# Kernel tuning notes

Measured on AMD Instinct MI355X. Metric: run time of the kernel, lower is better.

## Reference

```python
import jax, jax.numpy as jnp
import numpy as np

B, S, D, H = 4, 2048, 256, 4
DH = D // H  # per-head dim (shared for q, k, v)


def setup_inputs() -> dict:
    key = jax.random.key(0)
    ks = jax.random.split(key, 10)
    scale = 1.0 / np.sqrt(D)
    return {
        "q": jax.random.normal(ks[0], (B, S, D), jnp.float32),
        "k": jax.random.normal(ks[1], (B, S, D), jnp.float32),
        "v": jax.random.normal(ks[2], (B, S, D), jnp.float32),
        "mask": jax.random.randint(ks[3], (B, S, S), 0, 2).astype(bool),
        # per-head query/key projections: [H, D, DH] (+ bias [H, DH])
        "Wq": jax.random.uniform(ks[4], (H, D, DH), jnp.float32, -scale, scale),
        "bq": jax.random.uniform(ks[5], (H, DH), jnp.float32, -scale, scale),
        "Wk": jax.random.uniform(ks[6], (H, D, DH), jnp.float32, -scale, scale),
        "bk": jax.random.uniform(ks[7], (H, DH), jnp.float32, -scale, scale),
        # shared value projection: [D, DH]
        "Wv": jax.random.uniform(ks[8], (D, DH), jnp.float32, -scale, scale),
        "bv": jnp.zeros((DH,), jnp.float32),
        # final projection (no bias): [DH, D]
        "Wf": jax.random.uniform(ks[9], (DH, D), jnp.float32, -scale, scale),
    }


def reference(q, k, v, mask, Wq, bq, Wk, bk, Wv, bv, Wf):
    # per-head projections (all heads at once): [B, H, S, DH]
    q_h = jnp.einsum("bsd,hde->bhse", q, Wq) + bq[None, :, None, :]
    k_h = jnp.einsum("bsd,hde->bhse", k, Wk) + bk[None, :, None, :]
    # shared value projection: [B, S, DH]
    v_p = v @ Wv + bv
    # scaled scores: [B, H, S, S]
    scores = jnp.einsum("bhse,bhte->bhst", q_h, k_h) / jnp.sqrt(
        jnp.asarray(DH, q_h.dtype)
    )
    scores = jnp.where(mask[:, None, :, :], jnp.asarray(-1e9, scores.dtype), scores)
    attn = jax.nn.softmax(scores, axis=-1)  # [B, H, S, S]
    # shared V for every head: [B, H, S, DH]
    heads = jnp.einsum("bhst,bte->bhse", attn, v_p)
    mean_head = heads.mean(axis=1)  # [B, S, DH]
    out = mean_head @ Wf  # [B, S, D]
    return out, attn
```

## Files before the change

### kernel.cpp

```cpp
#include <hip/hip_runtime.h>
#include <stdint.h>
#include <stddef.h>

#define B_ 4
#define S_ 2048
#define D_ 256
#define H_ 4
#define DH_ 64
#define NT 128
#define SC_LOG2E 0.18033688011112042f

typedef __attribute__((ext_vector_type(8))) short short8;
typedef __attribute__((ext_vector_type(4))) short short4v;
typedef __attribute__((ext_vector_type(4))) float f32x4;
typedef unsigned int uint;

__device__ __forceinline__ short bf16_rne(float f) {
  union { float f; uint32_t u; } c; c.f = f;
  uint32_t u = c.u + 0x7FFFu + ((c.u >> 16) & 1u);
  return (short)(u >> 16);
}

__device__ __forceinline__ f32x4 mfma16(short8 a, short8 b, f32x4 c) {
  return __builtin_amdgcn_mfma_f32_16x16x32_bf16(a, b, c, 0, 0, 0);
}

__device__ __forceinline__ void gl_lds16(const short* g, short* l) {
  __builtin_amdgcn_global_load_lds(
      (const __attribute__((address_space(1))) unsigned int*)g,
      (__attribute__((address_space(3))) unsigned int*)l, 16, 0, 0);
}

__global__ void prep_weights(const float* __restrict__ Wq, const float* __restrict__ Wk,
                             const float* __restrict__ Wv,
                             short* __restrict__ WqT, short* __restrict__ WkT,
                             short* __restrict__ WvT) {
  int tid = blockIdx.x * blockDim.x + threadIdx.x;
  if (tid < 65536) {
    int n = tid >> 8, d = tid & 255;
    int hh = n >> 6, e = n & 63;
    WqT[tid] = bf16_rne(Wq[((size_t)hh * D_ + d) * DH_ + e]);
    WkT[tid] = bf16_rne(Wk[((size_t)hh * D_ + d) * DH_ + e]);
  } else if (tid < 65536 + 16384) {
    int t2 = tid - 65536;
    int e = t2 >> 8, d = t2 & 255;
    WvT[t2] = bf16_rne(Wv[(size_t)d * DH_ + e]);
  }
}

__global__ void detect_kernel(const unsigned int* __restrict__ m, int* __restrict__ flag) {
  __shared__ int isbool;
  if (threadIdx.x == 0) isbool = 0;
  __syncthreads();
#pragma unroll
  for (int i = 0; i < 4; ++i) {
    unsigned int d = m[threadIdx.x + i * 256];
    if (d & 0xFFFFFFFEu) isbool = 1;
  }
  __syncthreads();
  if (threadIdx.x == 0) *flag = isbool ? 0 : 1;
}

__global__ __launch_bounds__(256) void pack_mask(const unsigned char* __restrict__ maskB,
                                                 const int* __restrict__ flagp,
                                                 uint* __restrict__ mbits) {
  int tid = blockIdx.x * 256 + threadIdx.x;
  uint w = 0;
  if (*flagp) {
    const uint4* p = (const uint4*)((const uint*)maskB + (size_t)tid * 32);
#pragma unroll
    for (int i = 0; i < 8; ++i) {
      uint4 d = p[i];
      w |= (d.x ? 1u : 0u) << (i * 4);
      w |= (d.y ? 1u : 0u) << (i * 4 + 1);
      w |= (d.z ? 1u : 0u) << (i * 4 + 2);
      w |= (d.w ? 1u : 0u) << (i * 4 + 3);
    }
  } else {
    const uint4* p = (const uint4*)(maskB + (size_t)tid * 32);
#pragma unroll
    for (int i = 0; i < 2; ++i) {
      uint4 d = p[i];
      const uint* dw = (const uint*)&d;
#pragma unroll
      for (int j = 0; j < 4; ++j) {
        uint x = dw[j];
        int base = i * 16 + j * 4;
        w |= ((x & 0x000000FFu) ? 1u : 0u) << (base);
        w |= ((x & 0x0000FF00u) ? 1u : 0u) << (base + 1);
        w |= ((x & 0x00FF0000u) ? 1u : 0u) << (base + 2);
        w |= ((x & 0xFF000000u) ? 1u : 0u) << (base + 3);
      }
    }
  }
  mbits[tid] = w;
}

__global__ __launch_bounds__(256) void proj_kernel(
    const float* __restrict__ X, const short* __restrict__ WT,
    const float* __restrict__ bias, short* __restrict__ outp, int vmode) {
  const int b = blockIdx.z;
  const int s0 = blockIdx.x * 64;
  const int n0 = blockIdx.y * 64;
  const int tid = threadIdx.x;
  const int wave = tid >> 6, lane = tid & 63;
  const int lr = lane & 15, lg = lane >> 4;

  const int arowi = s0 + wave * 16 + lr;
  const float* xr = X + ((size_t)b * S_ + arowi) * D_;

  f32x4 zero4 = {0.f, 0.f, 0.f, 0.f};
  f32x4 acc[4];
#pragma unroll
  for (int ct = 0; ct < 4; ++ct) acc[ct] = zero4;

#pragma unroll
  for (int c = 0; c < 8; ++c) {
    const int k0 = c * 32 + lg * 8;
    f32x4 x0 = *(const f32x4*)(xr + k0);
    f32x4 x1 = *(const f32x4*)(xr + k0 + 4);
    short8 a;
#pragma unroll
    for (int jj = 0; jj < 4; ++jj) { a[jj] = bf16_rne(x0[jj]); a[4 + jj] = bf16_rne(x1[jj]); }
#pragma unroll
    for (int ct = 0; ct < 4; ++ct) {
      short8 bw = *(const short8*)(WT + (size_t)(n0 + ct * 16 + lr) * D_ + k0);
      acc[ct] = mfma16(a, bw, acc[ct]);
    }
  }

  if (vmode == 0) {
#pragma unroll
    for (int ct = 0; ct < 4; ++ct) {
      int n = n0 + ct * 16 + lr;
      float bb = bias[n];
      int hh = n >> 6, e = n & 63;
#pragma unroll
      for (int r = 0; r < 4; ++r) {
        int srow = s0 + wave * 16 + lg * 4 + r;
        outp[(((size_t)b * H_ + hh) * S_ + srow) * DH_ + e] = bf16_rne(acc[ct][r] + bb);
      }
    }
  } else {
#pragma unroll
    for (int ct = 0; ct < 4; ++ct) {
      int n = n0 + ct * 16 + lr;
      float bb = bias[n];
      int s4 = s0 + wave * 16 + lg * 4;
      short4v pk;
#pragma unroll
      for (int r = 0; r < 4; ++r) pk[r] = bf16_rne(acc[ct][r] + bb);
      *(short4v*)(outp + ((size_t)b * DH_ + n) * S_ + s4) = pk;
    }
  }
}

__device__ __forceinline__ void stageK(const short* Ksrc, short* dst, int wave, int lane) {
#pragma unroll
  for (int i = 0; i < 4; ++i) {
    int db = i * 256 + wave * 64;
    int d = db + lane;
    int s = (d & ~7) | ((d ^ (d >> 3)) & 7);
    gl_lds16(Ksrc + (size_t)s * 8, dst + (size_t)db * 8);
  }
}

__device__ __forceinline__ void stageV(const short* Vb, int t0, short* dst, int wave, int lane) {
#pragma unroll
  for (int i = 0; i < 4; ++i) {
    int db = i * 256 + wave * 64;
    int d = db + lane;
    int s = (d & ~15) | ((d ^ (d >> 4)) & 15);
    int er = s >> 4, c16 = s & 15;
    gl_lds16(Vb + (size_t)er * S_ + t0 + c16 * 8, dst + (size_t)db * 8);
  }
}

__global__ __launch_bounds__(256) void attn_kernel(
    const short* __restrict__ qh, const short* __restrict__ kh,
    const short* __restrict__ vT, const uint* __restrict__ mbits,
    float* __restrict__ attn, float* __restrict__ heads) {
  __shared__ __align__(16) short Kt[2][NT][DH_];
  __shared__ __align__(16) short Vt[2][DH_][NT];
  __shared__ __align__(16) short Pt[4][16][NT];

  const int flat = blockIdx.x;
  const int xcd = flat & 7;
  const int pos = flat >> 3;
  const int bh_i = xcd * 2 + (pos >> 5);
  const int q0 = (pos & 31) * 64;
  const int b = bh_i >> 2, h = bh_i & 3;

  const int tid = threadIdx.x;
  const int wave = tid >> 6, lane = tid & 63;
  const int lr = lane & 15, lg = lane >> 4;

  const size_t bh = (size_t)b * H_ + h;
  const short* Qb = qh + bh * S_ * DH_;
  const short* Kb = kh + bh * S_ * DH_;
  const short* Vb = vT + (size_t)b * DH_ * S_;

  const int qrow = q0 + wave * 16 + lr;
  const uint* mrow = mbits + ((size_t)b * S_ + qrow) * (S_ / 32);
  float* arow = attn + (bh * S_ + qrow) * S_;

  short8 aq0 = *(const short8*)(Qb + (size_t)qrow * DH_ + lg * 8);
  short8 aq1 = *(const short8*)(Qb + (size_t)qrow * DH_ + 32 + lg * 8);

  short* pw = &Pt[wave][0][0];

  float rsum = 0.f;
  stageK(Kb, &Kt[0][0][0], wave, lane);
  __syncthreads();
  int cur = 0;
  for (int t0 = 0; t0 < S_; t0 += NT) {
    if (t0 + NT < S_) stageK(Kb + (size_t)(t0 + NT) * DH_, &Kt[cur ^ 1][0][0], wave, lane);
    const short* kt = &Kt[cur][0][0];
    uint4 mv = *(const uint4*)(mrow + (t0 >> 5));
#pragma unroll
    for (int j = 0; j < 8; ++j) {
      int row = j * 16 + lr;
      int rs = row & 7;
      short8 bk0 = *(const short8*)(kt + row * 64 + ((lg ^ rs) * 8));
      short8 bk1 = *(const short8*)(kt + row * 64 + (((lg + 4) ^ rs) * 8));
      f32x4 acc = {0.f, 0.f, 0.f, 0.f};
      acc = mfma16(bk0, aq0, acc);
      acc = mfma16(bk1, aq1, acc);
      uint mw = ((const uint*)&mv)[j >> 1];
#pragma unroll
      for (int r = 0; r < 4; ++r) {
        int sh = (j & 1) * 16 + lg * 4 + r;
        float p = ((mw >> sh) & 1u) ? 0.f : __builtin_exp2f(acc[r] * SC_LOG2E);
        rsum += p;
      }
    }
    __syncthreads();
    cur ^= 1;
  }
  rsum += __shfl_xor(rsum, 16);
  rsum += __shfl_xor(rsum, 32);
  const float rinv = 1.0f / rsum;

  f32x4 o[4];
#pragma unroll
  for (int ct = 0; ct < 4; ++ct) o[ct] = (f32x4){0.f, 0.f, 0.f, 0.f};

  stageK(Kb, &Kt[0][0][0], wave, lane);
  stageV(Vb, 0, &Vt[0][0][0], wave, lane);
  __syncthreads();
  cur = 0;
  for (int t0 = 0; t0 < S_; t0 += NT) {
    if (t0 + NT < S_) {
      stageK(Kb + (size_t)(t0 + NT) * DH_, &Kt[cur ^ 1][0][0], wave, lane);
      stageV(Vb, t0 + NT, &Vt[cur ^ 1][0][0], wave, lane);
    }
    const short* kt = &Kt[cur][0][0];
    const short* vt = &Vt[cur][0][0];
    uint4 mv = *(const uint4*)(mrow + (t0 >> 5));
#pragma unroll
    for (int j = 0; j < 8; ++j) {
      int row = j * 16 + lr;
      int rs = row & 7;
      short8 bk0 = *(const short8*)(kt + row * 64 + ((lg ^ rs) * 8));
      short8 bk1 = *(const short8*)(kt + row * 64 + (((lg + 4) ^ rs) * 8));
      f32x4 acc = {0.f, 0.f, 0.f, 0.f};
      acc = mfma16(bk0, aq0, acc);
      acc = mfma16(bk1, aq1, acc);
      uint mw = ((const uint*)&mv)[j >> 1];
      f32x4 pst;
      short4v pk;
#pragma unroll
      for (int r = 0; r < 4; ++r) {
        int sh = (j & 1) * 16 + lg * 4 + r;
        float p = ((mw >> sh) & 1u) ? 0.f : __builtin_exp2f(acc[r] * SC_LOG2E) * rinv;
        pst[r] = p;
        pk[r] = bf16_rne(p);
      }
      *(f32x4*)(arow + t0 + j * 16 + lg * 4) = pst;
      int slot = j * 2 + (lg >> 1);
      *(short4v*)(pw + lr * 128 + ((slot ^ lr) * 8) + (lg & 1) * 4) = pk;
    }
#pragma unroll
    for (int ct = 0; ct < 4; ++ct) {
#pragma unroll
      for (int kc = 0; kc < 4; ++kc) {
        short8 apf = *(const short8*)(pw + lr * 128 + (((kc * 4 + lg) ^ lr) * 8));
        int er = ct * 16 + lr;
        short8 bvf = *(const short8*)(vt + er * 128 + (((kc * 4 + lg) ^ (er & 15)) * 8));
        o[ct] = mfma16(bvf, apf, o[ct]);
      }
    }
    __syncthreads();
    cur ^= 1;
  }

#pragma unroll
  for (int ct = 0; ct < 4; ++ct)
    *(f32x4*)(heads + (bh * S_ + qrow) * DH_ + ct * 16 + lg * 4) = o[ct];
}

__global__ __launch_bounds__(256) void final_kernel(
    const float* __restrict__ heads, const float* __restrict__ Wf,
    float* __restrict__ outp) {
  __shared__ float mean[16][DH_];
  const int row0 = blockIdx.x * 16;
  const int tid = threadIdx.x;
#pragma unroll
  for (int i = 0; i < 4; ++i) {
    int idx = tid + i * 256;
    int r = idx >> 6, e = idx & 63;
    int gs = row0 + r;
    int bb = gs >> 11, ss = gs & (S_ - 1);
    float acc = 0.f;
#pragma unroll
    for (int hh = 0; hh < H_; ++hh)
      acc += heads[(((size_t)bb * H_ + hh) * S_ + ss) * DH_ + e];
    mean[r][e] = acc * 0.25f;
  }
  __syncthreads();
  float acc[16];
#pragma unroll
  for (int r = 0; r < 16; ++r) acc[r] = 0.f;
  for (int e = 0; e < DH_; ++e) {
    float wf = Wf[(size_t)e * D_ + tid];
#pragma unroll
    for (int r = 0; r < 16; ++r) acc[r] += mean[r][e] * wf;
  }
#pragma unroll
  for (int r = 0; r < 16; ++r)
    outp[(size_t)(row0 + r) * D_ + tid] = acc[r];
}

extern "C" void kernel_launch(void* const* d_in, const int* in_sizes, int n_in,
                              void* d_out, int out_size, void* d_ws, size_t ws_size,
                              hipStream_t stream) {
  (void)in_sizes; (void)n_in; (void)out_size; (void)ws_size;
  const float* q  = (const float*)d_in[0];
  const float* k  = (const float*)d_in[1];
  const float* v  = (const float*)d_in[2];
  const unsigned char* mask = (const unsigned char*)d_in[3];
  const float* Wq = (const float*)d_in[4];
  const float* bq = (const float*)d_in[5];
  const float* Wk = (const float*)d_in[6];
  const float* bk = (const float*)d_in[7];
  const float* Wv = (const float*)d_in[8];
  const float* bv = (const float*)d_in[9];
  const float* Wf = (const float*)d_in[10];

  float* out  = (float*)d_out;
  float* attn = out + (size_t)B_ * S_ * D_;

  char* ws = (char*)d_ws;
  short* qh    = (short*)(ws);
  short* kh    = (short*)(ws + 4194304);
  short* vT    = (short*)(ws + 8388608);
  short* WqT   = (short*)(ws + 9437184);
  short* WkT   = (short*)(ws + 9568256);
  short* WvT   = (short*)(ws + 9699328);
  float* heads = (float*)(ws + 9732096);
  int*   flag  = (int*)(ws + 18120704);
  uint*  mbits = (uint*)(ws + 18120768);

  detect_kernel<<<1, 256, 0, stream>>>((const unsigned int*)mask, flag);
  pack_mask<<<2048, 256, 0, stream>>>(mask, flag, mbits);
  prep_weights<<<320, 256, 0, stream>>>(Wq, Wk, Wv, WqT, WkT, WvT);
  proj_kernel<<<dim3(32, 4, B_), 256, 0, stream>>>(q, WqT, bq, qh, 0);
  proj_kernel<<<dim3(32, 4, B_), 256, 0, stream>>>(k, WkT, bk, kh, 0);
  proj_kernel<<<dim3(32, 1, B_), 256, 0, stream>>>(v, WvT, bv, vT, 1);
  attn_kernel<<<512, 256, 0, stream>>>(qh, kh, vT, mbits, attn, heads);
  final_kernel<<<512, 256, 0, stream>>>(heads, Wf, out);
}
```

Measured before the change: 182.7 us.

## Split attention key range across two wave groups and fold softmax scale into Wq

The attention kernel now launches 512 threads per block. Two groups of four waves each handle one half of the key sequence with 64-wide tiles, then combine their row sums and output accumulators through LDS. The softmax scale times log2(e) is folded into the Q weights and bias, which removes one multiply per score. This raises the number of waves per query block, giving more latency hiding for the exp and global attention-write work, at the cost of extra syncs and an LDS reduction. Rounding Q to bf16 after the scale is applied slightly changes numerics.

```diff
diff --git a/kernel.cpp b/kernel.cpp
--- a/kernel.cpp
+++ b/kernel.cpp
@@ -7,7 +7,7 @@
 #define D_ 256
 #define H_ 4
 #define DH_ 64
-#define NT 128
+#define NTT 64
 #define SC_LOG2E 0.18033688011112042f
 
 typedef __attribute__((ext_vector_type(8))) short short8;
@@ -39,7 +39,7 @@
   if (tid < 65536) {
     int n = tid >> 8, d = tid & 255;
     int hh = n >> 6, e = n & 63;
-    WqT[tid] = bf16_rne(Wq[((size_t)hh * D_ + d) * DH_ + e]);
+    WqT[tid] = bf16_rne(Wq[((size_t)hh * D_ + d) * DH_ + e] * SC_LOG2E);
     WkT[tid] = bf16_rne(Wk[((size_t)hh * D_ + d) * DH_ + e]);
   } else if (tid < 65536 + 16384) {
     int t2 = tid - 65536;
@@ -98,7 +98,7 @@
 
 __global__ __launch_bounds__(256) void proj_kernel(
     const float* __restrict__ X, const short* __restrict__ WT,
-    const float* __restrict__ bias, short* __restrict__ outp, int vmode) {
+    const float* __restrict__ bias, short* __restrict__ outp, int vmode, float bscale) {
   const int b = blockIdx.z;
   const int s0 = blockIdx.x * 64;
   const int n0 = blockIdx.y * 64;
@@ -133,7 +133,7 @@
 #pragma unroll
     for (int ct = 0; ct < 4; ++ct) {
       int n = n0 + ct * 16 + lr;
-      float bb = bias[n];
+      float bb = bias[n] * bscale;
       int hh = n >> 6, e = n & 63;
 #pragma unroll
       for (int r = 0; r < 4; ++r) {
@@ -155,34 +155,33 @@
   }
 }
 
-__device__ __forceinline__ void stageK(const short* Ksrc, short* dst, int wave, int lane) {
-#pragma unroll
-  for (int i = 0; i < 4; ++i) {
-    int db = i * 256 + wave * 64;
-    int d = db + lane;
-    int s = (d & ~7) | ((d ^ (d >> 3)) & 7);
-    gl_lds16(Ksrc + (size_t)s * 8, dst + (size_t)db * 8);
-  }
-}
-
-__device__ __forceinline__ void stageV(const short* Vb, int t0, short* dst, int wave, int lane) {
-#pragma unroll
-  for (int i = 0; i < 4; ++i) {
-    int db = i * 256 + wave * 64;
-    int d = db + lane;
-    int s = (d & ~15) | ((d ^ (d >> 4)) & 15);
-    int er = s >> 4, c16 = s & 15;
-    gl_lds16(Vb + (size_t)er * S_ + t0 + c16 * 8, dst + (size_t)db * 8);
-  }
-}
-
-__global__ __launch_bounds__(256) void attn_kernel(
+__device__ __forceinline__ void stageK64(const short* Ksrc, short* dst, int wq, int lane) {
+#pragma unroll
+  for (int i = 0; i < 2; ++i) {
+    int ub = i * 256 + wq * 64;
+    int u = ub + lane;
+    int row = u >> 3, c = (u ^ row) & 7;
+    gl_lds16(Ksrc + (size_t)row * 64 + c * 8, dst + (size_t)ub * 8);
+  }
+}
+
+__device__ __forceinline__ void stageV64(const short* Vb, int t0, short* dst, int wq, int lane) {
+#pragma unroll
+  for (int i = 0; i < 2; ++i) {
+    int ub = i * 256 + wq * 64;
+    int u = ub + lane;
+    int er = u >> 3, c = (u ^ er) & 7;
+    gl_lds16(Vb + (size_t)er * S_ + t0 + c * 8, dst + (size_t)ub * 8);
+  }
+}
+
+__global__ __launch_bounds__(512, 4) void attn_kernel(
     const short* __restrict__ qh, const short* __restrict__ kh,
     const short* __restrict__ vT, const uint* __restrict__ mbits,
     float* __restrict__ attn, float* __restrict__ heads) {
-  __shared__ __align__(16) short Kt[2][NT][DH_];
-  __shared__ __align__(16) short Vt[2][DH_][NT];
-  __shared__ __align__(16) short Pt[4][16][NT];
+  __shared__ __align__(16) short Kt[2][2][4096];
+  __shared__ __align__(16) short Vt[2][2][4096];
+  __shared__ __align__(16) short Pt[8][1024];
 
   const int flat = blockIdx.x;
   const int xcd = flat & 7;
@@ -193,44 +192,46 @@
 
   const int tid = threadIdx.x;
   const int wave = tid >> 6, lane = tid & 63;
+  const int half = wave >> 2, wq = wave & 3;
   const int lr = lane & 15, lg = lane >> 4;
+  const int tbase = half * (S_ / 2);
 
   const size_t bh = (size_t)b * H_ + h;
   const short* Qb = qh + bh * S_ * DH_;
   const short* Kb = kh + bh * S_ * DH_;
   const short* Vb = vT + (size_t)b * DH_ * S_;
 
-  const int qrow = q0 + wave * 16 + lr;
+  const int qrow = q0 + wq * 16 + lr;
   const uint* mrow = mbits + ((size_t)b * S_ + qrow) * (S_ / 32);
   float* arow = attn + (bh * S_ + qrow) * S_;
 
-  short8 aq0 = *(const short8*)(Qb + (size_t)qrow * DH_ + lg * 8);
-  short8 aq1 = *(const short8*)(Qb + (size_t)qrow * DH_ + 32 + lg * 8);
-
-  short* pw = &Pt[wave][0][0];
+  const short8 aq0 = *(const short8*)(Qb + (size_t)qrow * DH_ + lg * 8);
+  const short8 aq1 = *(const short8*)(Qb + (size_t)qrow * DH_ + 32 + lg * 8);
+
+  short* pw = &Pt[wave][0];
 
   float rsum = 0.f;
-  stageK(Kb, &Kt[0][0][0], wave, lane);
+  stageK64(Kb + (size_t)tbase * DH_, Kt[half][0], wq, lane);
   __syncthreads();
   int cur = 0;
-  for (int t0 = 0; t0 < S_; t0 += NT) {
-    if (t0 + NT < S_) stageK(Kb + (size_t)(t0 + NT) * DH_, &Kt[cur ^ 1][0][0], wave, lane);
-    const short* kt = &Kt[cur][0][0];
-    uint4 mv = *(const uint4*)(mrow + (t0 >> 5));
-#pragma unroll
-    for (int j = 0; j < 8; ++j) {
+  for (int tt = 0; tt < 16; ++tt) {
+    const int t0 = tbase + tt * NTT;
+    if (tt + 1 < 16) stageK64(Kb + (size_t)(t0 + NTT) * DH_, Kt[half][cur ^ 1], wq, lane);
+    const short* kt = Kt[half][cur];
+    uint2 mv = *(const uint2*)(mrow + (t0 >> 5));
+#pragma unroll
+    for (int j = 0; j < 4; ++j) {
       int row = j * 16 + lr;
-      int rs = row & 7;
-      short8 bk0 = *(const short8*)(kt + row * 64 + ((lg ^ rs) * 8));
-      short8 bk1 = *(const short8*)(kt + row * 64 + (((lg + 4) ^ rs) * 8));
+      short8 bk0 = *(const short8*)(kt + row * 64 + (((lg) ^ row) & 7) * 8);
+      short8 bk1 = *(const short8*)(kt + row * 64 + (((lg + 4) ^ row) & 7) * 8);
       f32x4 acc = {0.f, 0.f, 0.f, 0.f};
       acc = mfma16(bk0, aq0, acc);
       acc = mfma16(bk1, aq1, acc);
-      uint mw = ((const uint*)&mv)[j >> 1];
+      uint mw = (j < 2) ? mv.x : mv.y;
 #pragma unroll
       for (int r = 0; r < 4; ++r) {
         int sh = (j & 1) * 16 + lg * 4 + r;
-        float p = ((mw >> sh) & 1u) ? 0.f : __builtin_exp2f(acc[r] * SC_LOG2E);
+        float p = ((mw >> sh) & 1u) ? 0.f : __builtin_exp2f(acc[r]);
         rsum += p;
       }
     }
@@ -239,64 +240,82 @@
   }
   rsum += __shfl_xor(rsum, 16);
   rsum += __shfl_xor(rsum, 32);
-  const float rinv = 1.0f / rsum;
+  float* fsum = (float*)&Pt[0][0];
+  if (lane < 16) fsum[wave * 16 + lr] = rsum;
+  __syncthreads();
+  const float rinv = 1.0f / (fsum[wq * 16 + lr] + fsum[(wq + 4) * 16 + lr]);
 
   f32x4 o[4];
 #pragma unroll
   for (int ct = 0; ct < 4; ++ct) o[ct] = (f32x4){0.f, 0.f, 0.f, 0.f};
 
-  stageK(Kb, &Kt[0][0][0], wave, lane);
-  stageV(Vb, 0, &Vt[0][0][0], wave, lane);
+  stageK64(Kb + (size_t)tbase * DH_, Kt[half][0], wq, lane);
+  stageV64(Vb, tbase, Vt[half][0], wq, lane);
   __syncthreads();
   cur = 0;
-  for (int t0 = 0; t0 < S_; t0 += NT) {
-    if (t0 + NT < S_) {
-      stageK(Kb + (size_t)(t0 + NT) * DH_, &Kt[cur ^ 1][0][0], wave, lane);
-      stageV(Vb, t0 + NT, &Vt[cur ^ 1][0][0], wave, lane);
-    }
-    const short* kt = &Kt[cur][0][0];
-    const short* vt = &Vt[cur][0][0];
-    uint4 mv = *(const uint4*)(mrow + (t0 >> 5));
-#pragma unroll
-    for (int j = 0; j < 8; ++j) {
+  for (int tt = 0; tt < 16; ++tt) {
+    const int t0 = tbase + tt * NTT;
+    if (tt + 1 < 16) {
+      stageK64(Kb + (size_t)(t0 + NTT) * DH_, Kt[half][cur ^ 1], wq, lane);
+      stageV64(Vb, t0 + NTT, Vt[half][cur ^ 1], wq, lane);
+    }
+    const short* kt = Kt[half][cur];
+    const short* vt = Vt[half][cur];
+    uint2 mv = *(const uint2*)(mrow + (t0 >> 5));
+#pragma unroll
+    for (int j = 0; j < 4; ++j) {
       int row = j * 16 + lr;
-      int rs = row & 7;
-      short8 bk0 = *(const short8*)(kt + row * 64 + ((lg ^ rs) * 8));
-      short8 bk1 = *(const short8*)(kt + row * 64 + (((lg + 4) ^ rs) * 8));
+      short8 bk0 = *(const short8*)(kt + row * 64 + (((lg) ^ row) & 7) * 8);
+      short8 bk1 = *(const short8*)(kt + row * 64 + (((lg + 4) ^ row) & 7) * 8);
       f32x4 acc = {0.f, 0.f, 0.f, 0.f};
       acc = mfma16(bk0, aq0, acc);
       acc = mfma16(bk1, aq1, acc);
-      uint mw = ((const uint*)&mv)[j >> 1];
+      uint mw = (j < 2) ? mv.x : mv.y;
       f32x4 pst;
       short4v pk;
 #pragma unroll
       for (int r = 0; r < 4; ++r) {
         int sh = (j & 1) * 16 + lg * 4 + r;
-        float p = ((mw >> sh) & 1u) ? 0.f : __builtin_exp2f(acc[r] * SC_LOG2E) * rinv;
+        float p = ((mw >> sh) & 1u) ? 0.f : __builtin_exp2f(acc[r]) * rinv;
         pst[r] = p;
         pk[r] = bf16_rne(p);
       }
       *(f32x4*)(arow + t0 + j * 16 + lg * 4) = pst;
-      int slot = j * 2 + (lg >> 1);
-      *(short4v*)(pw + lr * 128 + ((slot ^ lr) * 8) + (lg & 1) * 4) = pk;
-    }
-#pragma unroll
-    for (int ct = 0; ct < 4; ++ct) {
-#pragma unroll
-      for (int kc = 0; kc < 4; ++kc) {
-        short8 apf = *(const short8*)(pw + lr * 128 + (((kc * 4 + lg) ^ lr) * 8));
-        int er = ct * 16 + lr;
-        short8 bvf = *(const short8*)(vt + er * 128 + (((kc * 4 + lg) ^ (er & 15)) * 8));
-        o[ct] = mfma16(bvf, apf, o[ct]);
+      *(short4v*)(pw + lr * 64 + (((2 * j + (lg >> 1)) ^ lr) & 7) * 8 + (lg & 1) * 4) = pk;
+    }
+    short8 apf[2];
+#pragma unroll
+    for (int kc = 0; kc < 2; ++kc)
+      apf[kc] = *(const short8*)(pw + lr * 64 + (((4 * kc + lg) ^ lr) & 7) * 8);
+#pragma unroll
+    for (int ct = 0; ct < 4; ++ct) {
+      int er = ct * 16 + lr;
+#pragma unroll
+      for (int kc = 0; kc < 2; ++kc) {
+        short8 bvf = *(const short8*)(vt + er * 64 + (((4 * kc + lg) ^ er) & 7) * 8);
+        o[ct] = mfma16(bvf, apf[kc], o[ct]);
       }
     }
     __syncthreads();
     cur ^= 1;
   }
 
-#pragma unroll
-  for (int ct = 0; ct < 4; ++ct)
-    *(f32x4*)(heads + (bh * S_ + qrow) * DH_ + ct * 16 + lg * 4) = o[ct];
+  float* ocomb = (float*)&Pt[0][0];
+  if (half == 1) {
+#pragma unroll
+    for (int ct = 0; ct < 4; ++ct)
+      *(f32x4*)(ocomb + wq * 1024 + lr * 64 + ct * 16 + lg * 4) = o[ct];
+  }
+  __syncthreads();
+  if (half == 0) {
+#pragma unroll
+    for (int ct = 0; ct < 4; ++ct) {
+      f32x4 t = *(const f32x4*)(ocomb + wq * 1024 + lr * 64 + ct * 16 + lg * 4);
+      f32x4 s = o[ct];
+      s[0] += t[0]; s[1] += t[1]; s[2] += t[2]; s[3] += t[3];
+      *(f32x4*)(heads + (bh * S_ + qrow) * DH_ + ct * 16 + lg * 4) = s;
+    }
+  }
 }
 
 __global__ __launch_bounds__(256) void final_kernel(
@@ -364,9 +383,9 @@
   detect_kernel<<<1, 256, 0, stream>>>((const unsigned int*)mask, flag);
   pack_mask<<<2048, 256, 0, stream>>>(mask, flag, mbits);
   prep_weights<<<320, 256, 0, stream>>>(Wq, Wk, Wv, WqT, WkT, WvT);
-  proj_kernel<<<dim3(32, 4, B_), 256, 0, stream>>>(q, WqT, bq, qh, 0);
-  proj_kernel<<<dim3(32, 4, B_), 256, 0, stream>>>(k, WkT, bk, kh, 0);
-  proj_kernel<<<dim3(32, 1, B_), 256, 0, stream>>>(v, WvT, bv, vT, 1);
-  attn_kernel<<<512, 256, 0, stream>>>(qh, kh, vT, mbits, attn, heads);
+  proj_kernel<<<dim3(32, 4, B_), 256, 0, stream>>>(q, WqT, bq, qh, 0, SC_LOG2E);
+  proj_kernel<<<dim3(32, 4, B_), 256, 0, stream>>>(k, WkT, bk, kh, 0, 1.0f);
+  proj_kernel<<<dim3(32, 1, B_), 256, 0, stream>>>(v, WvT, bv, vT, 1, 1.0f);
+  attn_kernel<<<512, 512, 0, stream>>>(qh, kh, vT, mbits, attn, heads);
   final_kernel<<<512, 256, 0, stream>>>(heads, Wf, out);
 }
```

Result: faster. 172.1 us (-5.8%).
